# Kernel tuning notes

Measured on AMD Instinct MI355X. Metric: run time of the kernel, lower is better.

## Reference

```python
import jax, jax.numpy as jnp
import numpy as np

H, DH = 8, 32  # heads, dim_head
DN, DE = 256, 128  # dim_node, dim_edge


def _ln(x, g, b, eps=1e-5):
    mu = jnp.mean(x, axis=-1, keepdims=True)
    var = jnp.var(x, axis=-1, keepdims=True)
    return (x - mu) * jax.lax.rsqrt(var + eps) * g + b


def setup_inputs() -> dict:
    key = jax.random.key(0)
    ks = jax.random.split(key, 12)
    b, r, w = 1, 128, 256
    s = 0.02
    return {
        "x": jax.random.normal(ks[0], (b, r, w, DN), jnp.float32),
        "edges": jax.random.normal(ks[1], (b, w, w, DE), jnp.float32),
        "mask": jax.random.bernoulli(ks[2], 0.9, (b, r, w)),
        "edge_mask": jax.random.bernoulli(ks[3], 0.9, (b, w, w)),
        "ln_g": jnp.ones((DN,), jnp.float32),
        "ln_b": jnp.zeros((DN,), jnp.float32),
        "lne_g": jnp.ones((DE,), jnp.float32),
        "lne_b": jnp.zeros((DE,), jnp.float32),
        "W_edge": jax.random.normal(ks[4], (DE, H), jnp.float32) * s,
        "Wq": jax.random.normal(ks[5], (DN, H * DH), jnp.float32) * s,
        "Wkv": jax.random.normal(ks[6], (DN, 2 * H * DH), jnp.float32) * s,
        "Wg": jax.random.normal(ks[7], (DN, H * DH), jnp.float32) * s,
        "bg": jnp.ones((H * DH,), jnp.float32),
        "Wo": jax.random.normal(ks[8], (H * DH, DN), jnp.float32) * s,
        "bo": jnp.zeros((DN,), jnp.float32),
    }


def reference(x, edges, mask, edge_mask, ln_g, ln_b, lne_g, lne_b,
              W_edge, Wq, Wkv, Wg, bg, Wo, bo):
    NEG = -jnp.finfo(x.dtype).max
    b, r, w, _ = x.shape
    xn = _ln(x, ln_g, ln_b)                       # pre-attn LayerNorm on nodes
    en = _ln(edges, lne_g, lne_b)                 # LayerNorm on edges
    bias = jnp.einsum('bije,eh->bhij', en, W_edge)  # edges -> per-head bias
    bias = jnp.where(edge_mask[:, None], bias, NEG)  # masked_fill on bias

    q = (xn @ Wq).reshape(b, r, w, H, DH)
    kv = xn @ Wkv
    k = kv[..., :H * DH].reshape(b, r, w, H, DH)
    v = kv[..., H * DH:].reshape(b, r, w, H, DH)
    scale = DH ** -0.5
    # row attention: rows act as extra batch dim; attend along width w
    dots = jnp.einsum('brihd,brjhd->brhij', q * scale, k) + bias[:, None]
    am = mask[:, :, None, :, None] & mask[:, :, None, None, :]  # [b,r,1,i,j]
    dots = jnp.where(am, dots, NEG)
    attn = jax.nn.softmax(dots, axis=-1)
    out = jnp.einsum('brhij,brjhd->brihd', attn, v).reshape(b, r, w, H * DH)
    gates = jax.nn.sigmoid(xn @ Wg + bg)          # gating on normed input
    out = out * gates
    return out @ Wo + bo
```

## Files before the change

### kernel.cpp

```cpp
#include <hip/hip_runtime.h>

#define NEGF (-3.402823466e38f)

constexpr int H  = 8,  DH = 32, DN = 256, DE = 128;
constexpr int RR = 128, WW = 256;
constexpr int MROWS = RR * WW;

typedef __attribute__((ext_vector_type(8))) short bf16x8;
typedef __attribute__((ext_vector_type(4))) short bf16x4;
typedef __attribute__((ext_vector_type(4))) float f32x4;

__device__ __forceinline__ float b2f(short s) {
  unsigned u = ((unsigned)(unsigned short)s) << 16;
  return __builtin_bit_cast(float, u);
}
__device__ __forceinline__ short f2b(float f) {
  unsigned u = __builtin_bit_cast(unsigned, f);
  unsigned r = (u + 0x7fffu + ((u >> 16) & 1u)) >> 16;
  return (short)r;
}
__device__ __forceinline__ float wred(float v) {
#pragma unroll
  for (int off = 32; off > 0; off >>= 1) v += __shfl_xor(v, off, 64);
  return v;
}

__global__ __launch_bounds__(256) void k_ln_x(const float* __restrict__ x,
                                              const float* __restrict__ g,
                                              const float* __restrict__ b,
                                              short* __restrict__ xnb) {
  const int wave = threadIdx.x >> 6, lane = threadIdx.x & 63;
  const int row = (blockIdx.x << 2) + wave;
  const float4 v = ((const float4*)(x + (size_t)row * DN))[lane];
  float s  = v.x + v.y + v.z + v.w;
  float s2 = v.x*v.x + v.y*v.y + v.z*v.z + v.w*v.w;
  s = wred(s); s2 = wred(s2);
  const float mu = s * (1.f / DN);
  const float rs = rsqrtf(s2 * (1.f / DN) - mu * mu + 1e-5f);
  const float4 gg = ((const float4*)g)[lane];
  const float4 bb = ((const float4*)b)[lane];
  bf16x4 o;
  o[0] = f2b((v.x - mu) * rs * gg.x + bb.x);
  o[1] = f2b((v.y - mu) * rs * gg.y + bb.y);
  o[2] = f2b((v.z - mu) * rs * gg.z + bb.z);
  o[3] = f2b((v.w - mu) * rs * gg.w + bb.w);
  ((bf16x4*)(xnb + (size_t)row * DN))[lane] = o;
}

__global__ __launch_bounds__(256) void k_prep(const float* __restrict__ Wq,
                                              const float* __restrict__ Wkv,
                                              const float* __restrict__ Wg,
                                              const float* __restrict__ Wo,
                                              short* __restrict__ wt) {
  const int idx = blockIdx.x * 256 + threadIdx.x;
  if (idx < 262144) {
    const int n = idx >> 8, k = idx & 255;
    float v;
    if (n < 256)      v = Wq[k * 256 + n];
    else if (n < 768) v = Wkv[k * 512 + (n - 256)];
    else              v = Wg[k * 256 + (n - 768)];
    wt[idx] = f2b(v);
  } else {
    const int m = idx - 262144;
    const int n = m >> 8, k = m & 255;
    wt[idx] = f2b(Wo[k * 256 + n]);
  }
}

__global__ __launch_bounds__(256) void k_bias(const float* __restrict__ edges,
                                              const int* __restrict__ emask,
                                              const float* __restrict__ g,
                                              const float* __restrict__ b,
                                              const float* __restrict__ We,
                                              float* __restrict__ bias2) {
  const int wave = threadIdx.x >> 6, lane = threadIdx.x & 63;
  const int p = (blockIdx.x << 2) + wave;
  const int i = p & (WW - 1), j = p >> 8;
  const float2 e = ((const float2*)(edges + (size_t)(i * WW + j) * DE))[lane];
  float s = e.x + e.y, s2 = e.x*e.x + e.y*e.y;
  s = wred(s); s2 = wred(s2);
  const float mu = s * (1.f / DE);
  const float rs = rsqrtf(s2 * (1.f / DE) - mu * mu + 1e-5f);
  const float2 gg = ((const float2*)g)[lane];
  const float2 bb = ((const float2*)b)[lane];
  const float n0 = (e.x - mu) * rs * gg.x + bb.x;
  const float n1 = (e.y - mu) * rs * gg.y + bb.y;
  const float* w0 = We + (lane * 2) * H;
  float acc[H];
#pragma unroll
  for (int h = 0; h < H; ++h) acc[h] = n0 * w0[h] + n1 * w0[H + h];
#pragma unroll
  for (int off = 32; off > 0; off >>= 1)
#pragma unroll
    for (int h = 0; h < H; ++h) acc[h] += __shfl_xor(acc[h], off, 64);
  if (lane == 0) {
    const int em = emask[i * WW + j];
#pragma unroll
    for (int h = 0; h < H; ++h)
      bias2[(size_t)((h << 6) + (j >> 2)) * 1024 + (i << 2) + (j & 3)]
          = em ? acc[h] : NEGF;
  }
}

template<int N, int EPI>
__global__ __launch_bounds__(256) void k_gemm(const short* __restrict__ A,
                                              const short* __restrict__ Bt,
                                              const float* __restrict__ bias,
                                              void* __restrict__ Cout) {
  __shared__ short As[128 * 64];
  __shared__ short Bs[128 * 64];
  const int tid = threadIdx.x;
  const int w = tid >> 6, lane = tid & 63;
  constexpr int nb = N / 128;
  const int bm = (blockIdx.x / nb) * 128;
  const int bn = (blockIdx.x % nb) * 128;
  const int wm = w >> 1, wn = w & 1;

  const int sr0 = (w << 5) + (lane >> 3);
  const int sc  = (lane & 7) << 3;

  f32x4 acc[4][4] = {};

  for (int k0 = 0; k0 < 256; k0 += 64) {
    __syncthreads();
#pragma unroll
    for (int q = 0; q < 4; ++q) {
      const int row = sr0 + (q << 3);
      const short* ga = A  + (size_t)(bm + row) * 256 + k0 + sc;
      const short* gb = Bt + (size_t)(bn + row) * 256 + k0 + sc;
      const int la = (w << 12) + (q << 10);
      __builtin_amdgcn_global_load_lds(
          (const __attribute__((address_space(1))) void*)ga,
          (__attribute__((address_space(3))) void*)((__attribute__((address_space(3))) char*)As + la),
          16, 0, 0);
      __builtin_amdgcn_global_load_lds(
          (const __attribute__((address_space(1))) void*)gb,
          (__attribute__((address_space(3))) void*)((__attribute__((address_space(3))) char*)Bs + la),
          16, 0, 0);
    }
    asm volatile("s_waitcnt vmcnt(0)" ::: "memory");
    __syncthreads();
#pragma unroll
    for (int ks = 0; ks < 2; ++ks) {
      const int kk = (ks << 5) + ((lane >> 4) << 3);
      bf16x8 af[4], bfr[4];
#pragma unroll
      for (int f = 0; f < 4; ++f) {
        const int ar = (wm << 6) + (f << 4) + (lane & 15);
        const int br = (wn << 6) + (f << 4) + (lane & 15);
        af[f]  = *(const bf16x8*)&As[ar * 64 + kk];
        bfr[f] = *(const bf16x8*)&Bs[br * 64 + kk];
      }
#pragma unroll
      for (int mi = 0; mi < 4; ++mi)
#pragma unroll
        for (int ni = 0; ni < 4; ++ni)
          acc[mi][ni] = __builtin_amdgcn_mfma_f32_16x16x32_bf16(
              af[mi], bfr[ni], acc[mi][ni], 0, 0, 0);
    }
  }

  const int r0 = bm + (wm << 6) + ((lane >> 4) << 2);
  const int c0 = bn + (wn << 6) + (lane & 15);
#pragma unroll
  for (int mi = 0; mi < 4; ++mi)
#pragma unroll
    for (int ni = 0; ni < 4; ++ni) {
      const int col = c0 + ni * 16;
      if (EPI == 0) {
        short* C = (short*)Cout;
        const bool gate = (bn + wn * 64 + ni * 16) >= 768;
        const float bgv = gate ? bias[col - 768] : 0.f;
#pragma unroll
        for (int jj = 0; jj < 4; ++jj) {
          float v = acc[mi][ni][jj];
          if (gate) v = 1.f / (1.f + __expf(-(v + bgv)));
          C[(size_t)(r0 + mi * 16 + jj) * N + col] = f2b(v);
        }
      } else {
        float* C = (float*)Cout;
        const float bv = bias[col];
#pragma unroll
        for (int jj = 0; jj < 4; ++jj)
          C[(size_t)(r0 + mi * 16 + jj) * N + col] = acc[mi][ni][jj] + bv;
      }
    }
}

__global__ __launch_bounds__(256) void k_attn(const short* __restrict__ qkvg,
                                              const float* __restrict__ bias2,
                                              const int* __restrict__ mask,
                                              short* __restrict__ aout) {
  __shared__ short K_lds[256 * 40];
  __shared__ short VT_lds[32 * 260];
  __shared__ float jm_lds[256];
  const int r = blockIdx.x >> 3, h = blockIdx.x & 7;
  const int tid = threadIdx.x;
  const int w = tid >> 6, lane = tid & 63;
  const int g = lane >> 4, c = lane & 15;
  const size_t rowbase = (size_t)r * WW;

  {
    const int jr = tid >> 2, ch = (tid & 3) << 3;
#pragma unroll
    for (int p = 0; p < 4; ++p) {
      const int j = (p << 6) + jr;
      const short* src = qkvg + (rowbase + j) * 1024 + 256 + h * 32 + ch;
      *(bf16x8*)&K_lds[j * 40 + ch] = *(const bf16x8*)src;
      const bf16x8 vv = *(const bf16x8*)(src + 256);
#pragma unroll
      for (int e = 0; e < 8; ++e) VT_lds[(ch + e) * 260 + j] = vv[e];
    }
    jm_lds[tid] = mask[r * WW + tid] ? 0.f : NEGF;
  }
  __syncthreads();

  const int q0 = (w << 6);
  bf16x8 qf[4];
  float qm[4];
#pragma unroll
  for (int qt = 0; qt < 4; ++qt) {
    qf[qt] = *(const bf16x8*)(qkvg + (rowbase + q0 + (qt << 4) + c) * 1024 + h * 32 + (g << 3));
    qm[qt] = jm_lds[q0 + (qt << 4) + c];
  }
  float m[4] = {NEGF, NEGF, NEGF, NEGF}, l[4] = {};
  f32x4 O[4][2] = {};
  const float scale = 0.17677669529663687f;
  const float* bh = bias2 + ((size_t)h << 16);

  for (int jb = 0; jb < WW; jb += 32) {
    const bf16x8 kf0 = *(const bf16x8*)&K_lds[(jb + c) * 40 + (g << 3)];
    const bf16x8 kf1 = *(const bf16x8*)&K_lds[(jb + 16 + c) * 40 + (g << 3)];
    const f32x4 jm0 = *(const f32x4*)&jm_lds[jb + (g << 2)];
    const f32x4 jm1 = *(const f32x4*)&jm_lds[jb + 16 + (g << 2)];
    f32x4 s[4][2];
    float pmax[4];
#pragma unroll
    for (int qt = 0; qt < 4; ++qt) {
      const f32x4 z = {0.f, 0.f, 0.f, 0.f};
      s[qt][0] = __builtin_amdgcn_mfma_f32_16x16x32_bf16(kf0, qf[qt], z, 0, 0, 0);
      s[qt][1] = __builtin_amdgcn_mfma_f32_16x16x32_bf16(kf1, qf[qt], z, 0, 0, 0);
      const int qq = q0 + (qt << 4) + c;
      const f32x4 bv0 = *(const f32x4*)(bh + (size_t)((jb >> 2) + (g)) * 1024 + (qq << 2));
      const f32x4 bv1 = *(const f32x4*)(bh + (size_t)((jb >> 2) + 4 + (g)) * 1024 + (qq << 2));
      float pm = NEGF;
#pragma unroll
      for (int rr = 0; rr < 4; ++rr) {
        float t0 = fmaxf(fmaf(s[qt][0][rr], scale, bv0[rr]) + jm0[rr] + qm[qt], NEGF);
        float t1 = fmaxf(fmaf(s[qt][1][rr], scale, bv1[rr]) + jm1[rr] + qm[qt], NEGF);
        s[qt][0][rr] = t0; s[qt][1][rr] = t1;
        pm = fmaxf(pm, fmaxf(t0, t1));
      }
      pm = fmaxf(pm, __shfl_xor(pm, 16, 64));
      pm = fmaxf(pm, __shfl_xor(pm, 32, 64));
      pmax[qt] = pm;
    }
    int need = 0;
#pragma unroll
    for (int qt = 0; qt < 4; ++qt) need |= (pmax[qt] > m[qt] + 8.f);
    if (__any(need)) {
      float fr[4];
#pragma unroll
      for (int qt = 0; qt < 4; ++qt) {
        const float mn = fmaxf(m[qt], pmax[qt]);
        fr[qt] = __expf(m[qt] - mn);
        m[qt] = mn; l[qt] *= fr[qt];
      }
#pragma unroll
      for (int qt = 0; qt < 4; ++qt)
#pragma unroll
        for (int rr = 0; rr < 4; ++rr) {
          const float fb = __shfl(fr[qt], (g << 2) | rr, 64);
          O[qt][0][rr] *= fb; O[qt][1][rr] *= fb;
        }
    }
    bf16x8 pa[4];
#pragma unroll
    for (int qt = 0; qt < 4; ++qt) {
      float sum = 0.f;
#pragma unroll
      for (int rr = 0; rr < 4; ++rr) {
        const float e0 = __expf(s[qt][0][rr] - m[qt]);
        const float e1 = __expf(s[qt][1][rr] - m[qt]);
        sum += e0 + e1;
        pa[qt][rr] = f2b(e0);
        pa[qt][rr + 4] = f2b(e1);
      }
      sum += __shfl_xor(sum, 16, 64);
      sum += __shfl_xor(sum, 32, 64);
      l[qt] += sum;
    }
    bf16x8 vf[2];
#pragma unroll
    for (int dt = 0; dt < 2; ++dt) {
      const int dd = (dt << 4) + c;
      const bf16x4 lo = *(const bf16x4*)&VT_lds[dd * 260 + jb + (g << 2)];
      const bf16x4 hi = *(const bf16x4*)&VT_lds[dd * 260 + jb + 16 + (g << 2)];
      vf[dt] = __builtin_shufflevector(lo, hi, 0, 1, 2, 3, 4, 5, 6, 7);
    }
#pragma unroll
    for (int qt = 0; qt < 4; ++qt)
#pragma unroll
      for (int dt = 0; dt < 2; ++dt)
        O[qt][dt] = __builtin_amdgcn_mfma_f32_16x16x32_bf16(pa[qt], vf[dt], O[qt][dt], 0, 0, 0);
  }

  float inv[4];
#pragma unroll
  for (int qt = 0; qt < 4; ++qt) inv[qt] = 1.f / l[qt];
#pragma unroll
  for (int qt = 0; qt < 4; ++qt)
#pragma unroll
    for (int rr = 0; rr < 4; ++rr) {
      const float iv = __shfl(inv[qt], (g << 2) | rr, 64);
      const size_t row = rowbase + q0 + (qt << 4) + (g << 2) + rr;
#pragma unroll
      for (int dt = 0; dt < 2; ++dt) {
        const int d = (dt << 4) + c;
        const float gate = b2f(qkvg[row * 1024 + 768 + h * 32 + d]);
        aout[row * 256 + h * 32 + d] = f2b(O[qt][dt][rr] * iv * gate);
      }
    }
}

extern "C" void kernel_launch(void* const* d_in, const int* in_sizes, int n_in,
                              void* d_out, int out_size, void* d_ws, size_t ws_size,
                              hipStream_t stream) {
  const float* x      = (const float*)d_in[0];
  const float* edges  = (const float*)d_in[1];
  const int*   mask   = (const int*)d_in[2];
  const int*   emask  = (const int*)d_in[3];
  const float* ln_g   = (const float*)d_in[4];
  const float* ln_b   = (const float*)d_in[5];
  const float* lne_g  = (const float*)d_in[6];
  const float* lne_b  = (const float*)d_in[7];
  const float* W_edge = (const float*)d_in[8];
  const float* Wq     = (const float*)d_in[9];
  const float* Wkv    = (const float*)d_in[10];
  const float* Wg     = (const float*)d_in[11];
  const float* bg     = (const float*)d_in[12];
  const float* Wo     = (const float*)d_in[13];
  const float* bo     = (const float*)d_in[14];
  float* out = (float*)d_out;

  char*  ws    = (char*)d_ws;
  short* qkvgb = (short*)ws;
  short* xnb   = (short*)(ws + 67108864);
  short* aoutb = (short*)(ws + 67108864 + 16777216);
  short* wt    = (short*)(ws + 100663296);
  float* bias2 = (float*)(ws + 101318656);

  k_ln_x<<<MROWS / 4, 256, 0, stream>>>(x, ln_g, ln_b, xnb);
  k_prep<<<1280, 256, 0, stream>>>(Wq, Wkv, Wg, Wo, wt);
  k_bias<<<(WW * WW) / 4, 256, 0, stream>>>(edges, emask, lne_g, lne_b, W_edge, bias2);
  k_gemm<1024, 0><<<(MROWS / 128) * 8, 256, 0, stream>>>(xnb, wt, bg, (void*)qkvgb);
  k_attn<<<RR * H, 256, 0, stream>>>(qkvgb, bias2, mask, aoutb);
  k_gemm<256, 1><<<(MROWS / 128) * 2, 256, 0, stream>>>(aoutb, wt + 262144, bo, (void*)out);
}
```

Measured before the change: 282.2 us.

## Restructure GEMM with full-K LDS B tile; use exp2 softmax and transposed V reads

The GEMM now stages the whole 128x256 B tile once into a swizzled LDS buffer and streams A fragments directly from global memory, with each wave computing 32x128 outputs. This removes the per-K-step LDS syncs at the cost of a larger 64KB LDS footprint and uncached A loads. The attention kernel folds log2(e) into the edge bias and the scale so it can use exp2, and stores V in a blocked layout read with ds_read_b64_tr_b16 transposed loads instead of scalar transposed stores. It also hoists the bias loads and unrolls the key loop by two.

```diff
diff --git a/kernel.cpp b/kernel.cpp
--- a/kernel.cpp
+++ b/kernel.cpp
@@ -1,6 +1,7 @@
 #include <hip/hip_runtime.h>
 
 #define NEGF (-3.402823466e38f)
+#define LOG2E 1.4426950408889634f
 
 constexpr int H  = 8,  DH = 32, DN = 256, DE = 128;
 constexpr int RR = 128, WW = 256;
@@ -9,6 +10,7 @@
 typedef __attribute__((ext_vector_type(8))) short bf16x8;
 typedef __attribute__((ext_vector_type(4))) short bf16x4;
 typedef __attribute__((ext_vector_type(4))) float f32x4;
+typedef __attribute__((ext_vector_type(2))) int i32x2;
 
 __device__ __forceinline__ float b2f(short s) {
   unsigned u = ((unsigned)(unsigned short)s) << 16;
@@ -98,7 +100,7 @@
 #pragma unroll
     for (int h = 0; h < H; ++h)
       bias2[(size_t)((h << 6) + (j >> 2)) * 1024 + (i << 2) + (j & 3)]
-          = em ? acc[h] : NEGF;
+          = em ? acc[h] * LOG2E : NEGF;
   }
 }
 
@@ -107,82 +109,72 @@
                                               const short* __restrict__ Bt,
                                               const float* __restrict__ bias,
                                               void* __restrict__ Cout) {
-  __shared__ short As[128 * 64];
-  __shared__ short Bs[128 * 64];
+  __shared__ short Bs[128 * 256];
   const int tid = threadIdx.x;
   const int w = tid >> 6, lane = tid & 63;
+  const int g = lane >> 4, c = lane & 15;
   constexpr int nb = N / 128;
-  const int bm = (blockIdx.x / nb) * 128;
-  const int bn = (blockIdx.x % nb) * 128;
-  const int wm = w >> 1, wn = w & 1;
-
-  const int sr0 = (w << 5) + (lane >> 3);
-  const int sc  = (lane & 7) << 3;
-
-  f32x4 acc[4][4] = {};
-
-  for (int k0 = 0; k0 < 256; k0 += 64) {
-    __syncthreads();
-#pragma unroll
-    for (int q = 0; q < 4; ++q) {
-      const int row = sr0 + (q << 3);
-      const short* ga = A  + (size_t)(bm + row) * 256 + k0 + sc;
-      const short* gb = Bt + (size_t)(bn + row) * 256 + k0 + sc;
-      const int la = (w << 12) + (q << 10);
-      __builtin_amdgcn_global_load_lds(
-          (const __attribute__((address_space(1))) void*)ga,
-          (__attribute__((address_space(3))) void*)((__attribute__((address_space(3))) char*)As + la),
-          16, 0, 0);
-      __builtin_amdgcn_global_load_lds(
-          (const __attribute__((address_space(1))) void*)gb,
-          (__attribute__((address_space(3))) void*)((__attribute__((address_space(3))) char*)Bs + la),
-          16, 0, 0);
-    }
-    asm volatile("s_waitcnt vmcnt(0)" ::: "memory");
-    __syncthreads();
-#pragma unroll
-    for (int ks = 0; ks < 2; ++ks) {
-      const int kk = (ks << 5) + ((lane >> 4) << 3);
-      bf16x8 af[4], bfr[4];
-#pragma unroll
-      for (int f = 0; f < 4; ++f) {
-        const int ar = (wm << 6) + (f << 4) + (lane & 15);
-        const int br = (wn << 6) + (f << 4) + (lane & 15);
-        af[f]  = *(const bf16x8*)&As[ar * 64 + kk];
-        bfr[f] = *(const bf16x8*)&Bs[br * 64 + kk];
-      }
-#pragma unroll
-      for (int mi = 0; mi < 4; ++mi)
-#pragma unroll
-        for (int ni = 0; ni < 4; ++ni)
-          acc[mi][ni] = __builtin_amdgcn_mfma_f32_16x16x32_bf16(
-              af[mi], bfr[ni], acc[mi][ni], 0, 0, 0);
-    }
-  }
-
-  const int r0 = bm + (wm << 6) + ((lane >> 4) << 2);
-  const int c0 = bn + (wn << 6) + (lane & 15);
-#pragma unroll
-  for (int mi = 0; mi < 4; ++mi)
-#pragma unroll
-    for (int ni = 0; ni < 4; ++ni) {
-      const int col = c0 + ni * 16;
+  const int bm = (int)(blockIdx.x / nb) * 128;
+  const int bn = (int)(blockIdx.x % nb) * 128;
+
+  const char* Bt_b = (const char*)(Bt + (size_t)bn * 256);
+#pragma unroll
+  for (int q = 0; q < 16; ++q) {
+    const int o = (q * 256 + tid) * 16;
+    const int osw = o ^ ((((o >> 9) & 7)) << 4);
+    __builtin_amdgcn_global_load_lds(
+        (const __attribute__((address_space(1))) void*)(Bt_b + osw),
+        (__attribute__((address_space(3))) void*)((__attribute__((address_space(3))) char*)Bs + o),
+        16, 0, 0);
+  }
+  asm volatile("s_waitcnt vmcnt(0)" ::: "memory");
+  __syncthreads();
+
+  const int m0 = bm + (w << 5);
+  f32x4 acc[2][8] = {};
+  const char* Bs_b = (const char*)Bs;
+#pragma unroll
+  for (int ks = 0; ks < 8; ++ks) {
+    bf16x8 af[2];
+#pragma unroll
+    for (int mi = 0; mi < 2; ++mi)
+      af[mi] = *(const bf16x8*)(A + (size_t)(m0 + (mi << 4) + c) * 256 + (ks << 5) + (g << 3));
+    bf16x8 bfr[8];
+#pragma unroll
+    for (int ni = 0; ni < 8; ++ni) {
+      const int L = ((ni << 4) + c) * 512 + (ks << 6) + (g << 4);
+      bfr[ni] = *(const bf16x8*)(Bs_b + (L ^ ((c & 7) << 4)));
+    }
+#pragma unroll
+    for (int mi = 0; mi < 2; ++mi)
+#pragma unroll
+      for (int ni = 0; ni < 8; ++ni)
+        acc[mi][ni] = __builtin_amdgcn_mfma_f32_16x16x32_bf16(af[mi], bfr[ni], acc[mi][ni], 0, 0, 0);
+  }
+
+  const int r0 = bm + (w << 5) + (g << 2);
+  const int c0 = bn + c;
+#pragma unroll
+  for (int mi = 0; mi < 2; ++mi)
+#pragma unroll
+    for (int ni = 0; ni < 8; ++ni) {
+      const int col = c0 + (ni << 4);
       if (EPI == 0) {
         short* C = (short*)Cout;
-        const bool gate = (bn + wn * 64 + ni * 16) >= 768;
+        const bool gate = (bn + (ni << 4)) >= 768;
         const float bgv = gate ? bias[col - 768] : 0.f;
 #pragma unroll
         for (int jj = 0; jj < 4; ++jj) {
           float v = acc[mi][ni][jj];
           if (gate) v = 1.f / (1.f + __expf(-(v + bgv)));
-          C[(size_t)(r0 + mi * 16 + jj) * N + col] = f2b(v);
+          C[(size_t)(r0 + (mi << 4) + jj) * N + col] = f2b(v);
         }
       } else {
         float* C = (float*)Cout;
         const float bv = bias[col];
 #pragma unroll
         for (int jj = 0; jj < 4; ++jj)
-          C[(size_t)(r0 + mi * 16 + jj) * N + col] = acc[mi][ni][jj] + bv;
+          C[(size_t)(r0 + (mi << 4) + jj) * N + col] = acc[mi][ni][jj] + bv;
       }
     }
 }
@@ -192,7 +184,7 @@
                                               const int* __restrict__ mask,
                                               short* __restrict__ aout) {
   __shared__ short K_lds[256 * 40];
-  __shared__ short VT_lds[32 * 260];
+  __shared__ alignas(16) short VS[8192];
   __shared__ float jm_lds[256];
   const int r = blockIdx.x >> 3, h = blockIdx.x & 7;
   const int tid = threadIdx.x;
@@ -202,14 +194,14 @@
 
   {
     const int jr = tid >> 2, ch = (tid & 3) << 3;
+    const int dt = ch >> 4, cc = ch & 15;
 #pragma unroll
     for (int p = 0; p < 4; ++p) {
       const int j = (p << 6) + jr;
       const short* src = qkvg + (rowbase + j) * 1024 + 256 + h * 32 + ch;
       *(bf16x8*)&K_lds[j * 40 + ch] = *(const bf16x8*)src;
-      const bf16x8 vv = *(const bf16x8*)(src + 256);
-#pragma unroll
-      for (int e = 0; e < 8; ++e) VT_lds[(ch + e) * 260 + j] = vv[e];
+      *(bf16x8*)&VS[(dt << 12) + ((j >> 2) << 6) + ((j & 3) << 4) + cc] =
+          *(const bf16x8*)(src + 256);
     }
     jm_lds[tid] = mask[r * WW + tid] ? 0.f : NEGF;
   }
@@ -225,14 +217,30 @@
   }
   float m[4] = {NEGF, NEGF, NEGF, NEGF}, l[4] = {};
   f32x4 O[4][2] = {};
-  const float scale = 0.17677669529663687f;
+  const float scale2 = 0.2550541611f;
   const float* bh = bias2 + ((size_t)h << 16);
-
+  const unsigned vs_base =
+      (unsigned)(uintptr_t)(__attribute__((address_space(3))) char*)VS;
+
+#pragma unroll 2
   for (int jb = 0; jb < WW; jb += 32) {
+    i32x2 vlo0, vhi0, vlo1, vhi1;
+    const unsigned va = vs_base + ((unsigned)(jb >> 2) << 7) + lane * 8;
+    asm volatile("ds_read_b64_tr_b16 %0, %1 offset:0"    : "=v"(vlo0) : "v"(va));
+    asm volatile("ds_read_b64_tr_b16 %0, %1 offset:512"  : "=v"(vhi0) : "v"(va));
+    asm volatile("ds_read_b64_tr_b16 %0, %1 offset:8192" : "=v"(vlo1) : "v"(va));
+    asm volatile("ds_read_b64_tr_b16 %0, %1 offset:8704" : "=v"(vhi1) : "v"(va));
     const bf16x8 kf0 = *(const bf16x8*)&K_lds[(jb + c) * 40 + (g << 3)];
     const bf16x8 kf1 = *(const bf16x8*)&K_lds[(jb + 16 + c) * 40 + (g << 3)];
     const f32x4 jm0 = *(const f32x4*)&jm_lds[jb + (g << 2)];
     const f32x4 jm1 = *(const f32x4*)&jm_lds[jb + 16 + (g << 2)];
+    f32x4 bv[4][2];
+#pragma unroll
+    for (int qt = 0; qt < 4; ++qt) {
+      const int qq = (q0 + (qt << 4) + c) << 2;
+      bv[qt][0] = *(const f32x4*)(bh + (size_t)((jb >> 2) + g) * 1024 + qq);
+      bv[qt][1] = *(const f32x4*)(bh + (size_t)((jb >> 2) + 4 + g) * 1024 + qq);
+    }
     f32x4 s[4][2];
     float pmax[4];
 #pragma unroll
@@ -240,14 +248,11 @@
       const f32x4 z = {0.f, 0.f, 0.f, 0.f};
       s[qt][0] = __builtin_amdgcn_mfma_f32_16x16x32_bf16(kf0, qf[qt], z, 0, 0, 0);
       s[qt][1] = __builtin_amdgcn_mfma_f32_16x16x32_bf16(kf1, qf[qt], z, 0, 0, 0);
-      const int qq = q0 + (qt << 4) + c;
-      const f32x4 bv0 = *(const f32x4*)(bh + (size_t)((jb >> 2) + (g)) * 1024 + (qq << 2));
-      const f32x4 bv1 = *(const f32x4*)(bh + (size_t)((jb >> 2) + 4 + (g)) * 1024 + (qq << 2));
       float pm = NEGF;
 #pragma unroll
       for (int rr = 0; rr < 4; ++rr) {
-        float t0 = fmaxf(fmaf(s[qt][0][rr], scale, bv0[rr]) + jm0[rr] + qm[qt], NEGF);
-        float t1 = fmaxf(fmaf(s[qt][1][rr], scale, bv1[rr]) + jm1[rr] + qm[qt], NEGF);
+        float t0 = fmaxf(fmaf(s[qt][0][rr], scale2, bv[qt][0][rr]) + jm0[rr] + qm[qt], NEGF);
+        float t1 = fmaxf(fmaf(s[qt][1][rr], scale2, bv[qt][1][rr]) + jm1[rr] + qm[qt], NEGF);
         s[qt][0][rr] = t0; s[qt][1][rr] = t1;
         pm = fmaxf(pm, fmaxf(t0, t1));
       }
@@ -257,13 +262,13 @@
     }
     int need = 0;
 #pragma unroll
-    for (int qt = 0; qt < 4; ++qt) need |= (pmax[qt] > m[qt] + 8.f);
+    for (int qt = 0; qt < 4; ++qt) need |= (pmax[qt] > m[qt] + 11.5416f);
     if (__any(need)) {
       float fr[4];
 #pragma unroll
       for (int qt = 0; qt < 4; ++qt) {
         const float mn = fmaxf(m[qt], pmax[qt]);
-        fr[qt] = __expf(m[qt] - mn);
+        fr[qt] = exp2f(m[qt] - mn);
         m[qt] = mn; l[qt] *= fr[qt];
       }
 #pragma unroll
@@ -280,8 +285,8 @@
       float sum = 0.f;
 #pragma unroll
       for (int rr = 0; rr < 4; ++rr) {
-        const float e0 = __expf(s[qt][0][rr] - m[qt]);
-        const float e1 = __expf(s[qt][1][rr] - m[qt]);
+        const float e0 = exp2f(s[qt][0][rr] - m[qt]);
+        const float e1 = exp2f(s[qt][1][rr] - m[qt]);
         sum += e0 + e1;
         pa[qt][rr] = f2b(e0);
         pa[qt][rr + 4] = f2b(e1);
@@ -290,19 +295,17 @@
       sum += __shfl_xor(sum, 32, 64);
       l[qt] += sum;
     }
-    bf16x8 vf[2];
-#pragma unroll
-    for (int dt = 0; dt < 2; ++dt) {
-      const int dd = (dt << 4) + c;
-      const bf16x4 lo = *(const bf16x4*)&VT_lds[dd * 260 + jb + (g << 2)];
-      const bf16x4 hi = *(const bf16x4*)&VT_lds[dd * 260 + jb + 16 + (g << 2)];
-      vf[dt] = __builtin_shufflevector(lo, hi, 0, 1, 2, 3, 4, 5, 6, 7);
-    }
-#pragma unroll
-    for (int qt = 0; qt < 4; ++qt)
-#pragma unroll
-      for (int dt = 0; dt < 2; ++dt)
-        O[qt][dt] = __builtin_amdgcn_mfma_f32_16x16x32_bf16(pa[qt], vf[dt], O[qt][dt], 0, 0, 0);
+    asm volatile("s_waitcnt lgkmcnt(0)" ::: "memory");
+    __builtin_amdgcn_sched_barrier(0);
+    const bf16x4 l0 = __builtin_bit_cast(bf16x4, vlo0), h0 = __builtin_bit_cast(bf16x4, vhi0);
+    const bf16x4 l1 = __builtin_bit_cast(bf16x4, vlo1), h1 = __builtin_bit_cast(bf16x4, vhi1);
+    const bf16x8 vf0 = __builtin_shufflevector(l0, h0, 0, 1, 2, 3, 4, 5, 6, 7);
+    const bf16x8 vf1 = __builtin_shufflevector(l1, h1, 0, 1, 2, 3, 4, 5, 6, 7);
+#pragma unroll
+    for (int qt = 0; qt < 4; ++qt) {
+      O[qt][0] = __builtin_amdgcn_mfma_f32_16x16x32_bf16(pa[qt], vf0, O[qt][0], 0, 0, 0);
+      O[qt][1] = __builtin_amdgcn_mfma_f32_16x16x32_bf16(pa[qt], vf1, O[qt][1], 0, 0, 0);
+    }
   }
 
   float inv[4];
@@ -353,7 +356,7 @@
   k_ln_x<<<MROWS / 4, 256, 0, stream>>>(x, ln_g, ln_b, xnb);
   k_prep<<<1280, 256, 0, stream>>>(Wq, Wkv, Wg, Wo, wt);
   k_bias<<<(WW * WW) / 4, 256, 0, stream>>>(edges, emask, lne_g, lne_b, W_edge, bias2);
-  k_gemm<1024, 0><<<(MROWS / 128) * 8, 256, 0, stream>>>(xnb, wt, bg, (void*)qkvgb);
+  k_gemm<1024, 0><<<256 * 8, 256, 0, stream>>>(xnb, wt, bg, (void*)qkvgb);
   k_attn<<<RR * H, 256, 0, stream>>>(qkvgb, bias2, mask, aoutb);
-  k_gemm<256, 1><<<(MROWS / 128) * 2, 256, 0, stream>>>(aoutb, wt + 262144, bo, (void*)out);
-}
+  k_gemm<256, 1><<<256 * 2, 256, 0, stream>>>(aoutb, wt + 262144, bo, (void*)out);
+}
```

Result: no change. 283.9 us (+0.6%).
